# Kernel optimization log

Measured on AMD Instinct MI355X. Metric: run time of the kernel, lower is better.

The kernel has to match this reference:

```python
import jax, jax.numpy as jnp
import numpy as np

WD, WH, WW = 2, 7, 7          # window size (D, H, W)
SD, SH, SW = 1, 3, 3          # shift size
DIM, NH = 128, 4              # channels, heads
B, D, H, W = 8, 8, 56, 56     # input dims
N = WD * WH * WW              # tokens per window = 98
HIDDEN = int(DIM * 4.0)


def _rel_index_np():
    coords = np.stack(np.meshgrid(np.arange(WD), np.arange(WH), np.arange(WW), indexing='ij'))
    coords = coords.reshape(3, -1)                      # [3, N]
    rel = (coords[:, :, None] - coords[:, None, :]).transpose(1, 2, 0)  # [N, N, 3]
    rel[:, :, 0] += WD - 1
    rel[:, :, 1] += WH - 1
    rel[:, :, 2] += WW - 1
    rel[:, :, 0] *= (2 * WH - 1) * (2 * WW - 1)
    rel[:, :, 1] *= (2 * WW - 1)
    return rel.sum(-1).astype(np.int32)                 # [N, N]


def _window_partition_np(x):
    b, d, h, w, c = x.shape
    x = x.reshape(b, d // WD, WD, h // WH, WH, w // WW, WW, c)
    return x.transpose(0, 1, 3, 5, 2, 4, 6, 7).reshape(-1, N, c)


def _attn_mask_np():
    img = np.zeros((1, D, H, W, 1), np.float32)
    cnt = 0
    for ds in (slice(0, -WD), slice(-WD, -SD), slice(-SD, None)):
        for hs in (slice(0, -WH), slice(-WH, -SH), slice(-SH, None)):
            for ws in (slice(0, -WW), slice(-WW, -SW), slice(-SW, None)):
                img[:, ds, hs, ws, :] = cnt
                cnt += 1
    mw = _window_partition_np(img).reshape(-1, N)       # [nW, N]
    am = mw[:, None, :] - mw[:, :, None]
    return np.where(am != 0, -100.0, 0.0).astype(np.float32)  # [nW, N, N]


def setup_inputs() -> dict:
    key = jax.random.key(0)
    ks = jax.random.split(key, 8)
    s = 0.02
    return {
        'x': jax.random.normal(ks[0], (B, D, H, W, DIM), jnp.float32),
        'mask_matrix': jnp.asarray(_attn_mask_np()),
        'rel_index': jnp.asarray(_rel_index_np()),
        'norm1_g': jnp.ones((DIM,), jnp.float32),
        'norm1_b': jnp.zeros((DIM,), jnp.float32),
        'qkv_w': s * jax.random.normal(ks[1], (DIM, 3 * DIM), jnp.float32),
        'qkv_b': jnp.zeros((3 * DIM,), jnp.float32),
        'rpb': s * jax.random.normal(ks[2], ((2 * WD - 1) * (2 * WH - 1) * (2 * WW - 1), NH), jnp.float32),
        'proj_w': s * jax.random.normal(ks[3], (DIM, DIM), jnp.float32),
        'proj_b': jnp.zeros((DIM,), jnp.float32),
        'norm2_g': jnp.ones((DIM,), jnp.float32),
        'norm2_b': jnp.zeros((DIM,), jnp.float32),
        'fc1_w': s * jax.random.normal(ks[4], (DIM, HIDDEN), jnp.float32),
        'fc1_b': jnp.zeros((HIDDEN,), jnp.float32),
        'fc2_w': s * jax.random.normal(ks[5], (HIDDEN, DIM), jnp.float32),
        'fc2_b': jnp.zeros((DIM,), jnp.float32),
    }


def _ln(x, g, b):
    mu = jnp.mean(x, -1, keepdims=True)
    v = jnp.mean((x - mu) ** 2, -1, keepdims=True)
    return (x - mu) * jax.lax.rsqrt(v + 1e-5) * g + b


def _partition(x):
    b, d, h, w, c = x.shape
    x = x.reshape(b, d // WD, WD, h // WH, WH, w // WW, WW, c)
    return x.transpose(0, 1, 3, 5, 2, 4, 6, 7).reshape(-1, N, c)


def _reverse(win, b, d, h, w):
    c = win.shape[-1]
    x = win.reshape(b, d // WD, h // WH, w // WW, WD, WH, WW, c)
    return x.transpose(0, 1, 4, 2, 5, 3, 6, 7).reshape(b, d, h, w, c)


def _forward(x, mask_matrix, rel_index, norm1_g, norm1_b, qkv_w, qkv_b, rpb,
             proj_w, proj_b, norm2_g, norm2_b, fc1_w, fc1_b, fc2_w, fc2_b):
    b, d, h, w, c = x.shape
    shortcut = x
    y = _ln(x, norm1_g, norm1_b)
    # pad to multiples of window size (static; 0 for chosen dims)
    pd, ph, pw = (-d) % WD, (-h) % WH, (-w) % WW
    y = jnp.pad(y, ((0, 0), (0, pd), (0, ph), (0, pw), (0, 0)))
    dp, hp, wp = d + pd, h + ph, w + pw
    # cyclic shift
    y = jnp.roll(y, (-SD, -SH, -SW), axis=(1, 2, 3))
    win = _partition(y)                                   # [Bw, N, C]
    bw = win.shape[0]
    hd = c // NH
    qkv = (win @ qkv_w + qkv_b).reshape(bw, N, 3, NH, hd).transpose(2, 0, 3, 1, 4)
    q, k, v = qkv[0] * (hd ** -0.5), qkv[1], qkv[2]       # [Bw, NH, N, hd]
    attn = jnp.einsum('bhnd,bhmd->bhnm', q, k)            # [Bw, NH, N, N]
    bias = rpb[rel_index].transpose(2, 0, 1)              # [NH, N, N]
    attn = attn + bias[None]
    nw = mask_matrix.shape[0]
    attn = attn.reshape(bw // nw, nw, NH, N, N) + mask_matrix[None, :, None]
    attn = jax.nn.softmax(attn.reshape(bw, NH, N, N), axis=-1)
    o = jnp.einsum('bhnm,bhmd->bhnd', attn, v).transpose(0, 2, 1, 3).reshape(bw, N, c)
    o = o @ proj_w + proj_b
    y = _reverse(o, b, dp, hp, wp)
    y = jnp.roll(y, (SD, SH, SW), axis=(1, 2, 3))[:, :d, :h, :w, :]
    x1 = shortcut + y                                     # first residual
    z = _ln(x1, norm2_g, norm2_b)
    z = jax.nn.gelu(z @ fc1_w + fc1_b, approximate=False)
    # NOTE: source code's call() returns drop_path(mlp(norm2(x))) WITHOUT the
    # second residual add; we replicate exactly (drop_path is Identity at rate 0).
    return z @ fc2_w + fc2_b


def reference(x, mask_matrix, rel_index, norm1_g, norm1_b, qkv_w, qkv_b, rpb,
              proj_w, proj_b, norm2_g, norm2_b, fc1_w, fc1_b, fc2_w, fc2_b):
    return _forward(x, mask_matrix, rel_index, norm1_g, norm1_b, qkv_w, qkv_b,
                    rpb, proj_w, proj_b, norm2_g, norm2_b, fc1_w, fc1_b, fc2_w, fc2_b)


if __name__ == '__main__':
    out = reference(**setup_inputs())
    print(out.shape)
```

## Files before the change

### kernel.cpp

```cpp
#include <hip/hip_runtime.h>
#include <hip/hip_bf16.h>

typedef __attribute__((ext_vector_type(8))) short bf16x8;
typedef __attribute__((ext_vector_type(4))) float f32x4;

#define MFMA(a,b,c) __builtin_amdgcn_mfma_f32_16x16x32_bf16((a),(b),(c),0,0,0)
#define WAVE_LDS_FENCE() do { asm volatile("s_waitcnt lgkmcnt(0)" ::: "memory"); \
                              __builtin_amdgcn_sched_barrier(0); } while (0)

static constexpr int NTOK = 8 * 8 * 56 * 56;
static constexpr int NT   = 98;
static constexpr int NWIN = 2048;
static constexpr int NN   = NT * NT;

__device__ __forceinline__ unsigned short f2bf(float f) {
  unsigned r;
  asm("v_cvt_pk_bf16_f32 %0, %1, %1" : "=v"(r) : "v"(f));
  return (unsigned short)r;
}
__device__ __forceinline__ unsigned f2bf2(float lo, float hi) {
  unsigned r;
  asm("v_cvt_pk_bf16_f32 %0, %1, %2" : "=v"(r) : "v"(lo), "v"(hi));
  return r;
}
__device__ __forceinline__ float bf2f(unsigned short s) {
  union { unsigned u; float f; } v; v.u = ((unsigned)s) << 16; return v.f;
}
union U8 { unsigned u[4]; bf16x8 v; };

__device__ __forceinline__ size_t srow_of(int t) {
  int widx = t / NT, n = t - widx * NT;
  int bb = widx >> 8, wb = widx & 255;
  int dW = wb >> 6, hW = (wb >> 3) & 7, wW = wb & 7;
  int dr = n / 49, rem = n - dr * 49, hr = rem / 7, wr = rem - hr * 7;
  int dsh = (dW * 2 + dr + 1) & 7;
  int hs = hW * 7 + hr + 3; if (hs >= 56) hs -= 56;
  int wsv = wW * 7 + wr + 3; if (wsv >= 56) wsv -= 56;
  return ((size_t)(bb * 8 + dsh) * 56 + hs) * 56 + wsv;
}

__global__ __launch_bounds__(256) void k0_prep(
    const float* __restrict__ qkv_w, const float* __restrict__ proj_w,
    const float* __restrict__ fc1_w, const float* __restrict__ fc2_w,
    const float* __restrict__ n1g, const float* __restrict__ n1b,
    const float* __restrict__ qkv_b,
    unsigned short* __restrict__ qkvT, unsigned short* __restrict__ projT,
    unsigned short* __restrict__ fc1T, unsigned short* __restrict__ fc2T,
    float* __restrict__ qbb) {
  int idx = blockIdx.x * 256 + threadIdx.x;
  if (idx < 384 * 128) { int n = idx >> 7, k = idx & 127; qkvT[idx] = f2bf(qkv_w[k * 384 + n] * n1g[k]); }
  if (idx < 128 * 128) { int n = idx >> 7, k = idx & 127; projT[idx] = f2bf(proj_w[k * 128 + n]); }
  if (idx < 512 * 128) { int n = idx >> 7, k = idx & 127; fc1T[idx] = f2bf(fc1_w[k * 512 + n]); }
  if (idx < 128 * 512) { int n = idx >> 9, k = idx & 511; fc2T[idx] = f2bf(fc2_w[k * 128 + n]); }
  if (idx < 384) {
    float acc = qkv_b[idx];
    for (int k = 0; k < 128; ++k) acc += n1b[k] * qkv_w[k * 384 + idx];
    qbb[idx] = acc;
  }
}

__global__ __launch_bounds__(256) void k0b_cmb(
    const int* __restrict__ rel, const float* __restrict__ rpb,
    const float* __restrict__ mask, unsigned short* __restrict__ cmb) {
  int idx = blockIdx.x * 256 + threadIdx.x;
  if (idx >= 4 * 8 * NN) return;
  int h = idx / (8 * NN);
  int rem = idx - h * 8 * NN;
  int cls = rem / NN, r = rem - cls * NN;
  int wb_rep = ((cls >> 2) & 1 ? 192 : 0) + ((cls >> 1) & 1 ? 56 : 0) + ((cls & 1) ? 7 : 0);
  cmb[idx] = f2bf(rpb[rel[r] * 4 + h] + mask[(size_t)wb_rep * NN + r]);
}

__global__ __launch_bounds__(256, 2) void k2_qkv(
    const float* __restrict__ x, const unsigned short* __restrict__ qkvT,
    const float* __restrict__ qbb,
    unsigned short* __restrict__ q, unsigned short* __restrict__ k,
    unsigned short* __restrict__ v) {
  __shared__ __align__(16) unsigned short wsW[64 * 136];
  int tid = threadIdx.x, wv = tid >> 6, lane = tid & 63;
  int l15 = lane & 15, lhi = lane >> 4;
  int mbase = blockIdx.x * 128 + wv * 32;

  bf16x8 afr[2][4];
#pragma unroll
  for (int mt = 0; mt < 2; ++mt) {
    int row = mbase + mt * 16 + l15;
    size_t srow = srow_of(row);
    const float* xr = x + srow * 128 + lhi * 8;
    float xv[4][8];
    float s = 0.f, ss = 0.f;
#pragma unroll
    for (int ks = 0; ks < 4; ++ks) {
      float4 lo = *(const float4*)(xr + ks * 32);
      float4 hi = *(const float4*)(xr + ks * 32 + 4);
      xv[ks][0] = lo.x; xv[ks][1] = lo.y; xv[ks][2] = lo.z; xv[ks][3] = lo.w;
      xv[ks][4] = hi.x; xv[ks][5] = hi.y; xv[ks][6] = hi.z; xv[ks][7] = hi.w;
#pragma unroll
      for (int e = 0; e < 8; ++e) { s += xv[ks][e]; ss += xv[ks][e] * xv[ks][e]; }
    }
    s += __shfl_xor(s, 16);  ss += __shfl_xor(ss, 16);
    s += __shfl_xor(s, 32);  ss += __shfl_xor(ss, 32);
    float mu = s * (1.f / 128.f);
    float var = ss * (1.f / 128.f) - mu * mu;
    float inv = __builtin_amdgcn_rsqf(var + 1e-5f);
#pragma unroll
    for (int ks = 0; ks < 4; ++ks) {
      U8 t;
#pragma unroll
      for (int p = 0; p < 4; ++p)
        t.u[p] = f2bf2((xv[ks][2 * p] - mu) * inv, (xv[ks][2 * p + 1] - mu) * inv);
      afr[mt][ks] = t.v;
    }
  }

  int rbase[2][4];
#pragma unroll
  for (int mt = 0; mt < 2; ++mt)
#pragma unroll
    for (int j = 0; j < 4; ++j) {
      int r = mbase + mt * 16 + lhi * 4 + j;
      int widx = r / NT, n = r - widx * NT;
      rbase[mt][j] = widx * 392 + n;
    }

  bf16x8 pf[4];
#pragma unroll
  for (int u = 0; u < 4; ++u) pf[u] = *(const bf16x8*)(qkvT + u * 2048 + tid * 8);

  for (int ch = 0; ch < 6; ++ch) {
#pragma unroll
    for (int u = 0; u < 4; ++u) {
      int flat = u * 2048 + tid * 8;
      *(bf16x8*)(&wsW[(flat >> 7) * 136 + (flat & 127)]) = pf[u];
    }
    __syncthreads();
    if (ch < 5) {
#pragma unroll
      for (int u = 0; u < 4; ++u)
        pf[u] = *(const bf16x8*)(qkvT + (ch + 1) * 8192 + u * 2048 + tid * 8);
    }
    f32x4 acc[2][4] = {};
#pragma unroll
    for (int ks = 0; ks < 4; ++ks)
#pragma unroll
      for (int nt = 0; nt < 4; ++nt) {
        bf16x8 bfr = *(const bf16x8*)(&wsW[(nt * 16 + l15) * 136 + ks * 32 + lhi * 8]);
#pragma unroll
        for (int mt = 0; mt < 2; ++mt)
          acc[mt][nt] = MFMA(afr[mt][ks], bfr, acc[mt][nt]);
      }
#pragma unroll
    for (int nt = 0; nt < 4; ++nt) {
      int col = ch * 64 + nt * 16 + l15;
      int which = col >> 7, head = (col >> 5) & 3, hd = col & 31;
      unsigned short* outb = which == 0 ? q : (which == 1 ? k : v);
      float scale = which == 0 ? 0.17677669529663687f : 1.0f;
      float bias = qbb[col];
#pragma unroll
      for (int mt = 0; mt < 2; ++mt)
#pragma unroll
        for (int j = 0; j < 4; ++j) {
          float val = (acc[mt][nt][j] + bias) * scale;
          outb[(size_t)(rbase[mt][j] + head * 98) * 32 + hd] = f2bf(val);
        }
    }
    __syncthreads();
  }
}

__global__ __launch_bounds__(512) void k3_attn(
    const unsigned short* __restrict__ q, const unsigned short* __restrict__ kk,
    const unsigned short* __restrict__ vv, const unsigned short* __restrict__ cmb,
    unsigned short* __restrict__ out) {
  __shared__ __align__(16) unsigned short Vt[32 * 140];
  __shared__ __align__(16) unsigned short Pw[7][16 * 140];
  int bid = blockIdx.x;
  int widx = bid >> 2, head = bid & 3;
  int wb = widx & 255;
  size_t base = (size_t)(widx * 4 + head) * NT * 32;
  int tid = threadIdx.x, wv = tid >> 6, lane = tid & 63;
  int l15 = lane & 15, lhi = lane >> 4;

  for (int idx = tid; idx < NT * 32; idx += 512) {
    int j = idx >> 5, d = idx & 31;
    Vt[d * 140 + j] = vv[base + idx];
  }
  for (int idx = tid; idx < 32 * 30; idx += 512) {
    int d = idx / 30, j = 98 + idx % 30;
    Vt[d * 140 + j] = 0;
  }
  __syncthreads();
  if (wv >= 7) return;

  int cls = (((wb >> 6) == 3) << 2) | ((((wb >> 3) & 7) == 7) << 1) | ((int)((wb & 7) == 7));
  const unsigned short* cw = cmb + ((size_t)(head * 8 + cls)) * NN;
  unsigned short* P = Pw[wv];
  int mb = wv * 16;

  bf16x8 afr = *(const bf16x8*)(q + base + (size_t)(mb + l15) * 32 + lhi * 8);
  f32x4 sfr[7];
#pragma unroll
  for (int nt = 0; nt < 7; ++nt) {
    bf16x8 bfr = *(const bf16x8*)(kk + base + (size_t)(nt * 16 + l15) * 32 + lhi * 8);
    f32x4 zz = {};
    sfr[nt] = MFMA(afr, bfr, zz);
  }
#pragma unroll
  for (int j = 0; j < 4; ++j) {
    int i = mb + lhi * 4 + j;
    int ic = i < 97 ? i : 97;
    float sv[7];
#pragma unroll
    for (int nt = 0; nt < 7; ++nt) {
      int colc = nt * 16 + l15;
      int jc = colc < 97 ? colc : 97;
      float s = fminf(fmaxf(sfr[nt][j], -1e4f), 1e4f);
      float bm = bf2f(cw[ic * NT + jc]);
      sv[nt] = (i < NT && colc < NT) ? (s + bm) : -1e30f;
    }
    float mx = sv[0];
#pragma unroll
    for (int nt = 1; nt < 7; ++nt) mx = fmaxf(mx, sv[nt]);
#pragma unroll
    for (int m2 = 1; m2 < 16; m2 <<= 1) mx = fmaxf(mx, __shfl_xor(mx, m2));
    float sum = 0.f, p[7];
#pragma unroll
    for (int nt = 0; nt < 7; ++nt) { p[nt] = __expf(sv[nt] - mx); sum += p[nt]; }
#pragma unroll
    for (int m2 = 1; m2 < 16; m2 <<= 1) sum += __shfl_xor(sum, m2);
    float inv = __builtin_amdgcn_rcpf(sum);
    int iloc = lhi * 4 + j;
#pragma unroll
    for (int nt = 0; nt < 7; ++nt)
      P[iloc * 140 + nt * 16 + l15] = f2bf(p[nt] * inv);
    P[iloc * 140 + 112 + l15] = 0;
  }
  WAVE_LDS_FENCE();

  f32x4 ofr[2] = {};
#pragma unroll
  for (int ks = 0; ks < 4; ++ks) {
    bf16x8 pafr = *(const bf16x8*)(P + l15 * 140 + ks * 32 + lhi * 8);
#pragma unroll
    for (int nt = 0; nt < 2; ++nt) {
      bf16x8 bfr = *(const bf16x8*)(Vt + (nt * 16 + l15) * 140 + ks * 32 + lhi * 8);
      ofr[nt] = MFMA(pafr, bfr, ofr[nt]);
    }
  }
#pragma unroll
  for (int nt = 0; nt < 2; ++nt)
#pragma unroll
    for (int j = 0; j < 4; ++j) {
      int n = mb + lhi * 4 + j;
      if (n < NT) {
        int d = nt * 16 + l15;
        out[(size_t)(widx * NT + n) * 128 + head * 32 + d] = f2bf(ofr[nt][j]);
      }
    }
}

__global__ __launch_bounds__(256, 3) void k4_proj_ln(
    const unsigned short* __restrict__ ao, const unsigned short* __restrict__ projT,
    const float* __restrict__ proj_b, const float* __restrict__ x,
    const float* __restrict__ g2, const float* __restrict__ b2,
    unsigned short* __restrict__ z) {
  __shared__ __align__(16) unsigned short wsW[128 * 136];
  int tid = threadIdx.x, wv = tid >> 6, lane = tid & 63;
  int l15 = lane & 15, lhi = lane >> 4;
  int mbase = blockIdx.x * 128 + wv * 32;

#pragma unroll
  for (int u = 0; u < 8; ++u) {
    int flat = u * 2048 + tid * 8;
    *(bf16x8*)(&wsW[(flat >> 7) * 136 + (flat & 127)]) = *(const bf16x8*)(projT + flat);
  }
  bf16x8 afr[2][4];
#pragma unroll
  for (int mt = 0; mt < 2; ++mt)
#pragma unroll
    for (int ks = 0; ks < 4; ++ks)
      afr[mt][ks] = *(const bf16x8*)(ao + (size_t)(mbase + mt * 16 + l15) * 128 + ks * 32 + lhi * 8);
  __syncthreads();

  f32x4 acc[2][8] = {};
#pragma unroll
  for (int ks = 0; ks < 4; ++ks)
#pragma unroll
    for (int nt = 0; nt < 8; ++nt) {
      bf16x8 bfr = *(const bf16x8*)(&wsW[(nt * 16 + l15) * 136 + ks * 32 + lhi * 8]);
#pragma unroll
      for (int mt = 0; mt < 2; ++mt)
        acc[mt][nt] = MFMA(afr[mt][ks], bfr, acc[mt][nt]);
    }
  __syncthreads();

  float* bounce = (float*)wsW + wv * (16 * 132);
  float pb[8];
#pragma unroll
  for (int nt = 0; nt < 8; ++nt) pb[nt] = proj_b[nt * 16 + l15];

  int rl = lane >> 2, c0 = (lane & 3) * 32;
#pragma unroll
  for (int mt = 0; mt < 2; ++mt) {
#pragma unroll
    for (int nt = 0; nt < 8; ++nt)
#pragma unroll
      for (int j = 0; j < 4; ++j)
        bounce[(lhi * 4 + j) * 132 + nt * 16 + l15] = acc[mt][nt][j] + pb[nt];
    WAVE_LDS_FENCE();

    int t = mbase + mt * 16 + rl;
    size_t srow = srow_of(t);
    const float* xr = x + srow * 128 + c0;
    float vals[32];
    float s = 0.f, ss = 0.f;
#pragma unroll
    for (int i = 0; i < 8; ++i) {
      float4 pv = *(const float4*)(bounce + rl * 132 + c0 + 4 * i);
      float4 xv = *(const float4*)(xr + 4 * i);
      float a0 = pv.x + xv.x, a1 = pv.y + xv.y, a2 = pv.z + xv.z, a3 = pv.w + xv.w;
      vals[4 * i] = a0; vals[4 * i + 1] = a1; vals[4 * i + 2] = a2; vals[4 * i + 3] = a3;
      s += a0 + a1 + a2 + a3;
      ss += a0 * a0 + a1 * a1 + a2 * a2 + a3 * a3;
    }
    s += __shfl_xor(s, 1);  ss += __shfl_xor(ss, 1);
    s += __shfl_xor(s, 2);  ss += __shfl_xor(ss, 2);
    float mu = s * (1.f / 128.f);
    float var = ss * (1.f / 128.f) - mu * mu;
    float inv = __builtin_amdgcn_rsqf(var + 1e-5f);
    unsigned pk[16];
#pragma unroll
    for (int i = 0; i < 8; ++i) {
      float4 g = *(const float4*)(g2 + c0 + 4 * i);
      float4 b = *(const float4*)(b2 + c0 + 4 * i);
      pk[2 * i]     = f2bf2((vals[4 * i]     - mu) * inv * g.x + b.x,
                            (vals[4 * i + 1] - mu) * inv * g.y + b.y);
      pk[2 * i + 1] = f2bf2((vals[4 * i + 2] - mu) * inv * g.z + b.z,
                            (vals[4 * i + 3] - mu) * inv * g.w + b.w);
    }
    unsigned* zp = (unsigned*)(z + srow * 128 + c0);
#pragma unroll
    for (int i = 0; i < 4; ++i)
      *(uint4*)(zp + 4 * i) = make_uint4(pk[4 * i], pk[4 * i + 1], pk[4 * i + 2], pk[4 * i + 3]);
    WAVE_LDS_FENCE();
  }
}

__global__ __launch_bounds__(256, 2) void k5_mlp(
    const unsigned short* __restrict__ z, const unsigned short* __restrict__ fc1T,
    const float* __restrict__ fc1_b, const unsigned short* __restrict__ fc2T,
    const float* __restrict__ fc2_b, float* __restrict__ out) {
  __shared__ __align__(16) unsigned short wsA[64 * 132];
  __shared__ __align__(16) unsigned short wsB[128 * 68];
  __shared__ __align__(16) unsigned short hl[4][32 * 70];
  int tid = threadIdx.x, wv = tid >> 6, lane = tid & 63;
  int l15 = lane & 15, lhi = lane >> 4;
  int mbase = blockIdx.x * 128 + wv * 32;
  unsigned short* hw = hl[wv];

  bf16x8 afr[2][4];
#pragma unroll
  for (int mt = 0; mt < 2; ++mt)
#pragma unroll
    for (int ks = 0; ks < 4; ++ks)
      afr[mt][ks] = *(const bf16x8*)(z + (size_t)(mbase + mt * 16 + l15) * 128 + ks * 32 + lhi * 8);

  bf16x8 pfA[4], pfB[4];
#pragma unroll
  for (int u = 0; u < 4; ++u) pfA[u] = *(const bf16x8*)(fc1T + u * 2048 + tid * 8);
#pragma unroll
  for (int u = 0; u < 4; ++u) {
    int flat = u * 2048 + tid * 8;
    pfB[u] = *(const bf16x8*)(fc2T + (size_t)(flat >> 6) * 512 + (flat & 63));
  }

  f32x4 oacc[2][8] = {};
  for (int ch = 0; ch < 8; ++ch) {
#pragma unroll
    for (int u = 0; u < 4; ++u) {
      int flat = u * 2048 + tid * 8;
      *(bf16x8*)(&wsA[(flat >> 7) * 132 + (flat & 127)]) = pfA[u];
      *(bf16x8*)(&wsB[(flat >> 6) * 68 + (flat & 63)]) = pfB[u];
    }
    __syncthreads();
    if (ch < 7) {
#pragma unroll
      for (int u = 0; u < 4; ++u)
        pfA[u] = *(const bf16x8*)(fc1T + (ch + 1) * 8192 + u * 2048 + tid * 8);
#pragma unroll
      for (int u = 0; u < 4; ++u) {
        int flat = u * 2048 + tid * 8;
        pfB[u] = *(const bf16x8*)(fc2T + (size_t)(flat >> 6) * 512 + (ch + 1) * 64 + (flat & 63));
      }
    }
    f32x4 hacc[2][4] = {};
#pragma unroll
    for (int ks = 0; ks < 4; ++ks)
#pragma unroll
      for (int nt = 0; nt < 4; ++nt) {
        bf16x8 bfr = *(const bf16x8*)(&wsA[(nt * 16 + l15) * 132 + ks * 32 + lhi * 8]);
#pragma unroll
        for (int mt = 0; mt < 2; ++mt)
          hacc[mt][nt] = MFMA(afr[mt][ks], bfr, hacc[mt][nt]);
      }
#pragma unroll
    for (int mt = 0; mt < 2; ++mt)
#pragma unroll
      for (int nt = 0; nt < 4; ++nt)
#pragma unroll
        for (int j = 0; j < 4; ++j) {
          int r = mt * 16 + lhi * 4 + j;
          int hcol = ch * 64 + nt * 16 + l15;
          float hv = hacc[mt][nt][j] + fc1_b[hcol];
          float targ = hv * (1.5957691216f + 0.0713548162f * hv * hv);
          float gv = hv * __builtin_amdgcn_rcpf(1.0f + __expf(-targ));
          hw[r * 70 + nt * 16 + l15] = f2bf(gv);
        }
    WAVE_LDS_FENCE();
#pragma unroll
    for (int ks = 0; ks < 2; ++ks) {
      bf16x8 a2[2];
#pragma unroll
      for (int mt = 0; mt < 2; ++mt)
        a2[mt] = *(const bf16x8*)(&hw[(mt * 16 + l15) * 70 + ks * 32 + lhi * 8]);
#pragma unroll
      for (int nt = 0; nt < 8; ++nt) {
        bf16x8 bfr = *(const bf16x8*)(&wsB[(nt * 16 + l15) * 68 + ks * 32 + lhi * 8]);
#pragma unroll
        for (int mt = 0; mt < 2; ++mt)
          oacc[mt][nt] = MFMA(a2[mt], bfr, oacc[mt][nt]);
      }
    }
    WAVE_LDS_FENCE();
    __syncthreads();
  }
#pragma unroll
  for (int mt = 0; mt < 2; ++mt)
#pragma unroll
    for (int nt = 0; nt < 8; ++nt)
#pragma unroll
      for (int j = 0; j < 4; ++j) {
        int r = mbase + mt * 16 + lhi * 4 + j;
        out[(size_t)r * 128 + nt * 16 + l15] = oacc[mt][nt][j] + fc2_b[nt * 16 + l15];
      }
}

extern "C" void kernel_launch(void* const* d_in, const int* in_sizes, int n_in,
                              void* d_out, int out_size, void* d_ws, size_t ws_size,
                              hipStream_t stream) {
  const float* x      = (const float*)d_in[0];
  const float* mask   = (const float*)d_in[1];
  const int*   rel    = (const int*)d_in[2];
  const float* n1g    = (const float*)d_in[3];
  const float* n1b    = (const float*)d_in[4];
  const float* qkv_w  = (const float*)d_in[5];
  const float* qkv_b  = (const float*)d_in[6];
  const float* rpb    = (const float*)d_in[7];
  const float* proj_w = (const float*)d_in[8];
  const float* proj_b = (const float*)d_in[9];
  const float* n2g    = (const float*)d_in[10];
  const float* n2b    = (const float*)d_in[11];
  const float* fc1_w  = (const float*)d_in[12];
  const float* fc1_b  = (const float*)d_in[13];
  const float* fc2_w  = (const float*)d_in[14];
  const float* fc2_b  = (const float*)d_in[15];
  float* out = (float*)d_out;

  char* ws = (char*)d_ws;
  const size_t SZ = (size_t)NTOK * 128 * 2;
  unsigned short* win   = (unsigned short*)(ws);
  unsigned short* qb    = (unsigned short*)(ws + SZ);
  unsigned short* kb    = (unsigned short*)(ws + 2 * SZ);
  unsigned short* vb    = (unsigned short*)(ws + 3 * SZ);
  unsigned short* qkvT  = (unsigned short*)(ws + 4 * SZ);
  unsigned short* projT = qkvT + 384 * 128;
  unsigned short* fc1T  = projT + 128 * 128;
  unsigned short* fc2T  = fc1T + 512 * 128;
  unsigned short* cmb   = fc2T + 128 * 512;
  float* qbb            = (float*)(cmb + (size_t)4 * 8 * NN);
  unsigned short* ao = win;
  unsigned short* zb = qb;

  k0_prep<<<256, 256, 0, stream>>>(qkv_w, proj_w, fc1_w, fc2_w, n1g, n1b, qkv_b,
                                   qkvT, projT, fc1T, fc2T, qbb);
  k0b_cmb<<<(4 * 8 * NN + 255) / 256, 256, 0, stream>>>(rel, rpb, mask, cmb);
  k2_qkv<<<NTOK / 128, 256, 0, stream>>>(x, qkvT, qbb, qb, kb, vb);
  k3_attn<<<NWIN * 4, 512, 0, stream>>>(qb, kb, vb, cmb, ao);
  k4_proj_ln<<<NTOK / 128, 256, 0, stream>>>(ao, projT, proj_b, x, n2g, n2b, zb);
  k5_mlp<<<NTOK / 128, 256, 0, stream>>>(zb, fc1T, fc1_b, fc2T, fc2_b, out);
}
```

Measured before the change: 355.5 us.

## Fuse projection+LayerNorm kernel with MLP kernel, keeping LN output in LDS

Merges the attention projection/residual/LayerNorm kernel with the MLP kernel so the normalized activations are passed through LDS into MFMA fragments instead of being written to and reread from a global bf16 buffer. The final output is staged through LDS and written in the original token order. It also folds the query scale into the qkv weights and bias during prep, and splits the GELU/fc2 step into halves. This saves a global round trip and a kernel launch, but the fused kernel uses more LDS and registers, and occupancy bounds drop from 3 to 2 blocks.

New measurement: 478.9 us. 34.7% more time.

```diff
diff --git a/kernel.cpp b/kernel.cpp
--- a/kernel.cpp
+++ b/kernel.cpp
@@ -48,14 +48,18 @@
     unsigned short* __restrict__ fc1T, unsigned short* __restrict__ fc2T,
     float* __restrict__ qbb) {
   int idx = blockIdx.x * 256 + threadIdx.x;
-  if (idx < 384 * 128) { int n = idx >> 7, k = idx & 127; qkvT[idx] = f2bf(qkv_w[k * 384 + n] * n1g[k]); }
+  if (idx < 384 * 128) {
+    int n = idx >> 7, k = idx & 127;
+    float sc = n < 128 ? 0.17677669529663687f : 1.0f;
+    qkvT[idx] = f2bf(qkv_w[k * 384 + n] * n1g[k] * sc);
+  }
   if (idx < 128 * 128) { int n = idx >> 7, k = idx & 127; projT[idx] = f2bf(proj_w[k * 128 + n]); }
   if (idx < 512 * 128) { int n = idx >> 7, k = idx & 127; fc1T[idx] = f2bf(fc1_w[k * 512 + n]); }
   if (idx < 128 * 512) { int n = idx >> 9, k = idx & 511; fc2T[idx] = f2bf(fc2_w[k * 128 + n]); }
   if (idx < 384) {
     float acc = qkv_b[idx];
     for (int k = 0; k < 128; ++k) acc += n1b[k] * qkv_w[k * 384 + idx];
-    qbb[idx] = acc;
+    qbb[idx] = acc * (idx < 128 ? 0.17677669529663687f : 1.0f);
   }
 }
 
@@ -154,13 +158,12 @@
       int col = ch * 64 + nt * 16 + l15;
       int which = col >> 7, head = (col >> 5) & 3, hd = col & 31;
       unsigned short* outb = which == 0 ? q : (which == 1 ? k : v);
-      float scale = which == 0 ? 0.17677669529663687f : 1.0f;
       float bias = qbb[col];
 #pragma unroll
       for (int mt = 0; mt < 2; ++mt)
 #pragma unroll
         for (int j = 0; j < 4; ++j) {
-          float val = (acc[mt][nt][j] + bias) * scale;
+          float val = acc[mt][nt][j] + bias;
           outb[(size_t)(rbase[mt][j] + head * 98) * 32 + hd] = f2bf(val);
         }
     }
@@ -259,27 +262,31 @@
     }
 }
 
-__global__ __launch_bounds__(256, 3) void k4_proj_ln(
+__global__ __launch_bounds__(256, 2) void k45_proj_mlp(
     const unsigned short* __restrict__ ao, const unsigned short* __restrict__ projT,
     const float* __restrict__ proj_b, const float* __restrict__ x,
     const float* __restrict__ g2, const float* __restrict__ b2,
-    unsigned short* __restrict__ z) {
-  __shared__ __align__(16) unsigned short wsW[128 * 136];
+    const unsigned short* __restrict__ fc1T, const float* __restrict__ fc1_b,
+    const unsigned short* __restrict__ fc2T, const float* __restrict__ fc2_b,
+    float* __restrict__ out) {
+  __shared__ __align__(16) char smem[52224];
   int tid = threadIdx.x, wv = tid >> 6, lane = tid & 63;
   int l15 = lane & 15, lhi = lane >> 4;
   int mbase = blockIdx.x * 128 + wv * 32;
-
+  int rl = lane >> 2, c0 = (lane & 3) * 32;
+
+  unsigned short* wsW = (unsigned short*)smem;
 #pragma unroll
   for (int u = 0; u < 8; ++u) {
     int flat = u * 2048 + tid * 8;
     *(bf16x8*)(&wsW[(flat >> 7) * 136 + (flat & 127)]) = *(const bf16x8*)(projT + flat);
   }
-  bf16x8 afr[2][4];
+  bf16x8 aofr[2][4];
 #pragma unroll
   for (int mt = 0; mt < 2; ++mt)
 #pragma unroll
     for (int ks = 0; ks < 4; ++ks)
-      afr[mt][ks] = *(const bf16x8*)(ao + (size_t)(mbase + mt * 16 + l15) * 128 + ks * 32 + lhi * 8);
+      aofr[mt][ks] = *(const bf16x8*)(ao + (size_t)(mbase + mt * 16 + l15) * 128 + ks * 32 + lhi * 8);
   __syncthreads();
 
   f32x4 acc[2][8] = {};
@@ -290,33 +297,36 @@
       bf16x8 bfr = *(const bf16x8*)(&wsW[(nt * 16 + l15) * 136 + ks * 32 + lhi * 8]);
 #pragma unroll
       for (int mt = 0; mt < 2; ++mt)
-        acc[mt][nt] = MFMA(afr[mt][ks], bfr, acc[mt][nt]);
+        acc[mt][nt] = MFMA(aofr[mt][ks], bfr, acc[mt][nt]);
     }
   __syncthreads();
 
-  float* bounce = (float*)wsW + wv * (16 * 132);
+  float* bounce = (float*)(smem + wv * 8704);
+  unsigned short* zt = (unsigned short*)(smem + wv * 8704);
   float pb[8];
 #pragma unroll
   for (int nt = 0; nt < 8; ++nt) pb[nt] = proj_b[nt * 16 + l15];
 
-  int rl = lane >> 2, c0 = (lane & 3) * 32;
+  bf16x8 afr[2][4];
+  size_t srows[2];
 #pragma unroll
   for (int mt = 0; mt < 2; ++mt) {
 #pragma unroll
     for (int nt = 0; nt < 8; ++nt)
 #pragma unroll
       for (int j = 0; j < 4; ++j)
-        bounce[(lhi * 4 + j) * 132 + nt * 16 + l15] = acc[mt][nt][j] + pb[nt];
+        bounce[(lhi * 4 + j) * 136 + nt * 16 + l15] = acc[mt][nt][j] + pb[nt];
     WAVE_LDS_FENCE();
 
     int t = mbase + mt * 16 + rl;
     size_t srow = srow_of(t);
+    srows[mt] = srow;
     const float* xr = x + srow * 128 + c0;
     float vals[32];
     float s = 0.f, ss = 0.f;
 #pragma unroll
     for (int i = 0; i < 8; ++i) {
-      float4 pv = *(const float4*)(bounce + rl * 132 + c0 + 4 * i);
+      float4 pv = *(const float4*)(bounce + rl * 136 + c0 + 4 * i);
       float4 xv = *(const float4*)(xr + 4 * i);
       float a0 = pv.x + xv.x, a1 = pv.y + xv.y, a2 = pv.z + xv.z, a3 = pv.w + xv.w;
       vals[4 * i] = a0; vals[4 * i + 1] = a1; vals[4 * i + 2] = a2; vals[4 * i + 3] = a3;
@@ -338,32 +348,16 @@
       pk[2 * i + 1] = f2bf2((vals[4 * i + 2] - mu) * inv * g.z + b.z,
                             (vals[4 * i + 3] - mu) * inv * g.w + b.w);
     }
-    unsigned* zp = (unsigned*)(z + srow * 128 + c0);
-#pragma unroll
-    for (int i = 0; i < 4; ++i)
-      *(uint4*)(zp + 4 * i) = make_uint4(pk[4 * i], pk[4 * i + 1], pk[4 * i + 2], pk[4 * i + 3]);
-    WAVE_LDS_FENCE();
-  }
-}
-
-__global__ __launch_bounds__(256, 2) void k5_mlp(
-    const unsigned short* __restrict__ z, const unsigned short* __restrict__ fc1T,
-    const float* __restrict__ fc1_b, const unsigned short* __restrict__ fc2T,
-    const float* __restrict__ fc2_b, float* __restrict__ out) {
-  __shared__ __align__(16) unsigned short wsA[64 * 132];
-  __shared__ __align__(16) unsigned short wsB[128 * 68];
-  __shared__ __align__(16) unsigned short hl[4][32 * 70];
-  int tid = threadIdx.x, wv = tid >> 6, lane = tid & 63;
-  int l15 = lane & 15, lhi = lane >> 4;
-  int mbase = blockIdx.x * 128 + wv * 32;
-  unsigned short* hw = hl[wv];
-
-  bf16x8 afr[2][4];
-#pragma unroll
-  for (int mt = 0; mt < 2; ++mt)
+    WAVE_LDS_FENCE();
+#pragma unroll
+    for (int i = 0; i < 16; ++i)
+      *(unsigned*)(zt + rl * 136 + c0 + 2 * i) = pk[i];
+    WAVE_LDS_FENCE();
 #pragma unroll
     for (int ks = 0; ks < 4; ++ks)
-      afr[mt][ks] = *(const bf16x8*)(z + (size_t)(mbase + mt * 16 + l15) * 128 + ks * 32 + lhi * 8);
+      afr[mt][ks] = *(const bf16x8*)(zt + l15 * 136 + ks * 32 + lhi * 8);
+    WAVE_LDS_FENCE();
+  }
 
   bf16x8 pfA[4], pfB[4];
 #pragma unroll
@@ -373,6 +367,11 @@
     int flat = u * 2048 + tid * 8;
     pfB[u] = *(const bf16x8*)(fc2T + (size_t)(flat >> 6) * 512 + (flat & 63));
   }
+  __syncthreads();
+
+  unsigned short* wsA = (unsigned short*)smem;
+  unsigned short* wsB = wsA + 64 * 132;
+  unsigned short* hw  = wsB + 128 * 68 + wv * (32 * 70);
 
   f32x4 oacc[2][8] = {};
   for (int ch = 0; ch < 8; ++ch) {
@@ -404,45 +403,55 @@
           hacc[mt][nt] = MFMA(afr[mt][ks], bfr, hacc[mt][nt]);
       }
 #pragma unroll
-    for (int mt = 0; mt < 2; ++mt)
-#pragma unroll
-      for (int nt = 0; nt < 4; ++nt)
-#pragma unroll
-        for (int j = 0; j < 4; ++j) {
-          int r = mt * 16 + lhi * 4 + j;
-          int hcol = ch * 64 + nt * 16 + l15;
-          float hv = hacc[mt][nt][j] + fc1_b[hcol];
-          float targ = hv * (1.5957691216f + 0.0713548162f * hv * hv);
-          float gv = hv * __builtin_amdgcn_rcpf(1.0f + __expf(-targ));
-          hw[r * 70 + nt * 16 + l15] = f2bf(gv);
+    for (int half = 0; half < 2; ++half) {
+#pragma unroll
+      for (int mt = 0; mt < 2; ++mt)
+#pragma unroll
+        for (int nt2 = 0; nt2 < 2; ++nt2) {
+          int nt = half * 2 + nt2;
+#pragma unroll
+          for (int j = 0; j < 4; ++j) {
+            int r = mt * 16 + lhi * 4 + j;
+            int hcol = ch * 64 + nt * 16 + l15;
+            float hv = hacc[mt][nt][j] + fc1_b[hcol];
+            float targ = hv * (1.5957691216f + 0.0713548162f * hv * hv);
+            float gv = hv * __builtin_amdgcn_rcpf(1.0f + __expf(-targ));
+            hw[r * 70 + nt * 16 + l15] = f2bf(gv);
+          }
         }
-    WAVE_LDS_FENCE();
-#pragma unroll
-    for (int ks = 0; ks < 2; ++ks) {
       bf16x8 a2[2];
 #pragma unroll
       for (int mt = 0; mt < 2; ++mt)
-        a2[mt] = *(const bf16x8*)(&hw[(mt * 16 + l15) * 70 + ks * 32 + lhi * 8]);
+        a2[mt] = *(const bf16x8*)(&hw[(mt * 16 + l15) * 70 + half * 32 + lhi * 8]);
 #pragma unroll
       for (int nt = 0; nt < 8; ++nt) {
-        bf16x8 bfr = *(const bf16x8*)(&wsB[(nt * 16 + l15) * 68 + ks * 32 + lhi * 8]);
+        bf16x8 bfr = *(const bf16x8*)(&wsB[(nt * 16 + l15) * 68 + half * 32 + lhi * 8]);
 #pragma unroll
         for (int mt = 0; mt < 2; ++mt)
           oacc[mt][nt] = MFMA(a2[mt], bfr, oacc[mt][nt]);
       }
     }
-    WAVE_LDS_FENCE();
     __syncthreads();
   }
-#pragma unroll
-  for (int mt = 0; mt < 2; ++mt)
+
+  float* ob = (float*)(smem + wv * 8704);
+  float fb[8];
+#pragma unroll
+  for (int nt = 0; nt < 8; ++nt) fb[nt] = fc2_b[nt * 16 + l15];
+#pragma unroll
+  for (int mt = 0; mt < 2; ++mt) {
 #pragma unroll
     for (int nt = 0; nt < 8; ++nt)
 #pragma unroll
-      for (int j = 0; j < 4; ++j) {
-        int r = mbase + mt * 16 + lhi * 4 + j;
-        out[(size_t)r * 128 + nt * 16 + l15] = oacc[mt][nt][j] + fc2_b[nt * 16 + l15];
-      }
+      for (int j = 0; j < 4; ++j)
+        ob[(lhi * 4 + j) * 136 + nt * 16 + l15] = oacc[mt][nt][j] + fb[nt];
+    WAVE_LDS_FENCE();
+    float* orow = out + srows[mt] * 128 + c0;
+#pragma unroll
+    for (int i = 0; i < 8; ++i)
+      *(float4*)(orow + 4 * i) = *(const float4*)(ob + rl * 136 + c0 + 4 * i);
+    WAVE_LDS_FENCE();
+  }
 }
 
 extern "C" void kernel_launch(void* const* d_in, const int* in_sizes, int n_in,
@@ -479,13 +488,12 @@
   unsigned short* cmb   = fc2T + 128 * 512;
   float* qbb            = (float*)(cmb + (size_t)4 * 8 * NN);
   unsigned short* ao = win;
-  unsigned short* zb = qb;
 
   k0_prep<<<256, 256, 0, stream>>>(qkv_w, proj_w, fc1_w, fc2_w, n1g, n1b, qkv_b,
                                    qkvT, projT, fc1T, fc2T, qbb);
   k0b_cmb<<<(4 * 8 * NN + 255) / 256, 256, 0, stream>>>(rel, rpb, mask, cmb);
   k2_qkv<<<NTOK / 128, 256, 0, stream>>>(x, qkvT, qbb, qb, kb, vb);
   k3_attn<<<NWIN * 4, 512, 0, stream>>>(qb, kb, vb, cmb, ao);
-  k4_proj_ln<<<NTOK / 128, 256, 0, stream>>>(ao, projT, proj_b, x, n2g, n2b, zb);
-  k5_mlp<<<NTOK / 128, 256, 0, stream>>>(zb, fc1T, fc1_b, fc2T, fc2_b, out);
-}
+  k45_proj_mlp<<<NTOK / 128, 256, 0, stream>>>(ao, projT, proj_b, x, n2g, n2b,
+                                               fc1T, fc1_b, fc2T, fc2_b, out);
+}
```

## Pre-permute bias+mask table for vector loads, fold q scale into weights, prefetch residual

Applied to the files above, without the earlier changes.

The combined relative-position-bias and mask table is rebuilt in a lane-major padded layout (98x128 per head/class), so each lane in the attention kernel loads its seven bias values with one 16-byte vector load instead of seven scattered scalar loads. The attention query scale is folded into the prepared QKV weights and bias, which removes a multiply per output in the QKV kernel. The projection+LayerNorm kernel now issues the residual x loads early, before the GEMM, to hide their latency. The cost is slightly larger bias storage and more registers held live in k4.

Measured after the change: 352.8 us. No clear change (-0.7%).

```diff
diff --git a/kernel.cpp b/kernel.cpp
--- a/kernel.cpp
+++ b/kernel.cpp
@@ -48,14 +48,18 @@
     unsigned short* __restrict__ fc1T, unsigned short* __restrict__ fc2T,
     float* __restrict__ qbb) {
   int idx = blockIdx.x * 256 + threadIdx.x;
-  if (idx < 384 * 128) { int n = idx >> 7, k = idx & 127; qkvT[idx] = f2bf(qkv_w[k * 384 + n] * n1g[k]); }
+  if (idx < 384 * 128) {
+    int n = idx >> 7, k = idx & 127;
+    float sc = n < 128 ? 0.17677669529663687f : 1.0f;
+    qkvT[idx] = f2bf(qkv_w[k * 384 + n] * n1g[k] * sc);
+  }
   if (idx < 128 * 128) { int n = idx >> 7, k = idx & 127; projT[idx] = f2bf(proj_w[k * 128 + n]); }
   if (idx < 512 * 128) { int n = idx >> 7, k = idx & 127; fc1T[idx] = f2bf(fc1_w[k * 512 + n]); }
   if (idx < 128 * 512) { int n = idx >> 9, k = idx & 511; fc2T[idx] = f2bf(fc2_w[k * 128 + n]); }
   if (idx < 384) {
     float acc = qkv_b[idx];
     for (int k = 0; k < 128; ++k) acc += n1b[k] * qkv_w[k * 384 + idx];
-    qbb[idx] = acc;
+    qbb[idx] = acc * (idx < 128 ? 0.17677669529663687f : 1.0f);
   }
 }
 
@@ -63,12 +67,20 @@
     const int* __restrict__ rel, const float* __restrict__ rpb,
     const float* __restrict__ mask, unsigned short* __restrict__ cmb) {
   int idx = blockIdx.x * 256 + threadIdx.x;
-  if (idx >= 4 * 8 * NN) return;
-  int h = idx / (8 * NN);
-  int rem = idx - h * 8 * NN;
-  int cls = rem / NN, r = rem - cls * NN;
-  int wb_rep = ((cls >> 2) & 1 ? 192 : 0) + ((cls >> 1) & 1 ? 56 : 0) + ((cls & 1) ? 7 : 0);
-  cmb[idx] = f2bf(rpb[rel[r] * 4 + h] + mask[(size_t)wb_rep * NN + r]);
+  if (idx >= 4 * 8 * 98 * 128) return;
+  int nt = idx & 7;
+  int l15 = (idx >> 3) & 15;
+  int rest = idx >> 7;
+  int i = rest % 98;
+  int hc = rest / 98;
+  int h = hc >> 3, cls = hc & 7;
+  int col = nt * 16 + l15;
+  float val = 0.f;
+  if (nt < 7 && col < 98) {
+    int wb_rep = ((cls >> 2) & 1 ? 192 : 0) + ((cls >> 1) & 1 ? 56 : 0) + ((cls & 1) ? 7 : 0);
+    val = rpb[rel[i * NT + col] * 4 + h] + mask[(size_t)wb_rep * NN + i * NT + col];
+  }
+  cmb[idx] = f2bf(val);
 }
 
 __global__ __launch_bounds__(256, 2) void k2_qkv(
@@ -154,13 +166,12 @@
       int col = ch * 64 + nt * 16 + l15;
       int which = col >> 7, head = (col >> 5) & 3, hd = col & 31;
       unsigned short* outb = which == 0 ? q : (which == 1 ? k : v);
-      float scale = which == 0 ? 0.17677669529663687f : 1.0f;
       float bias = qbb[col];
 #pragma unroll
       for (int mt = 0; mt < 2; ++mt)
 #pragma unroll
         for (int j = 0; j < 4; ++j) {
-          float val = (acc[mt][nt][j] + bias) * scale;
+          float val = acc[mt][nt][j] + bias;
           outb[(size_t)(rbase[mt][j] + head * 98) * 32 + hd] = f2bf(val);
         }
     }
@@ -193,7 +204,7 @@
   if (wv >= 7) return;
 
   int cls = (((wb >> 6) == 3) << 2) | ((((wb >> 3) & 7) == 7) << 1) | ((int)((wb & 7) == 7));
-  const unsigned short* cw = cmb + ((size_t)(head * 8 + cls)) * NN;
+  const unsigned short* cw = cmb + (size_t)(head * 8 + cls) * 98 * 128;
   unsigned short* P = Pw[wv];
   int mb = wv * 16;
 
@@ -209,13 +220,13 @@
   for (int j = 0; j < 4; ++j) {
     int i = mb + lhi * 4 + j;
     int ic = i < 97 ? i : 97;
+    bf16x8 cv = *(const bf16x8*)(cw + ic * 128 + l15 * 8);
     float sv[7];
 #pragma unroll
     for (int nt = 0; nt < 7; ++nt) {
       int colc = nt * 16 + l15;
-      int jc = colc < 97 ? colc : 97;
       float s = fminf(fmaxf(sfr[nt][j], -1e4f), 1e4f);
-      float bm = bf2f(cw[ic * NT + jc]);
+      float bm = bf2f((unsigned short)cv[nt]);
       sv[nt] = (i < NT && colc < NT) ? (s + bm) : -1e30f;
     }
     float mx = sv[0];
@@ -268,6 +279,15 @@
   int tid = threadIdx.x, wv = tid >> 6, lane = tid & 63;
   int l15 = lane & 15, lhi = lane >> 4;
   int mbase = blockIdx.x * 128 + wv * 32;
+  int rl = lane >> 2, c0 = (lane & 3) * 32;
+
+  size_t srows[2];
+  srows[0] = srow_of(mbase + rl);
+  srows[1] = srow_of(mbase + 16 + rl);
+  float4 x0[8];
+#pragma unroll
+  for (int i = 0; i < 8; ++i)
+    x0[i] = *(const float4*)(x + srows[0] * 128 + c0 + 4 * i);
 
 #pragma unroll
   for (int u = 0; u < 8; ++u) {
@@ -294,12 +314,16 @@
     }
   __syncthreads();
 
+  float4 x1[8];
+#pragma unroll
+  for (int i = 0; i < 8; ++i)
+    x1[i] = *(const float4*)(x + srows[1] * 128 + c0 + 4 * i);
+
   float* bounce = (float*)wsW + wv * (16 * 132);
   float pb[8];
 #pragma unroll
   for (int nt = 0; nt < 8; ++nt) pb[nt] = proj_b[nt * 16 + l15];
 
-  int rl = lane >> 2, c0 = (lane & 3) * 32;
 #pragma unroll
   for (int mt = 0; mt < 2; ++mt) {
 #pragma unroll
@@ -309,15 +333,13 @@
         bounce[(lhi * 4 + j) * 132 + nt * 16 + l15] = acc[mt][nt][j] + pb[nt];
     WAVE_LDS_FENCE();
 
-    int t = mbase + mt * 16 + rl;
-    size_t srow = srow_of(t);
-    const float* xr = x + srow * 128 + c0;
+    size_t srow = srows[mt];
     float vals[32];
     float s = 0.f, ss = 0.f;
 #pragma unroll
     for (int i = 0; i < 8; ++i) {
       float4 pv = *(const float4*)(bounce + rl * 132 + c0 + 4 * i);
-      float4 xv = *(const float4*)(xr + 4 * i);
+      float4 xv = mt == 0 ? x0[i] : x1[i];
       float a0 = pv.x + xv.x, a1 = pv.y + xv.y, a2 = pv.z + xv.z, a3 = pv.w + xv.w;
       vals[4 * i] = a0; vals[4 * i + 1] = a1; vals[4 * i + 2] = a2; vals[4 * i + 3] = a3;
       s += a0 + a1 + a2 + a3;
@@ -477,13 +499,13 @@
   unsigned short* fc1T  = projT + 128 * 128;
   unsigned short* fc2T  = fc1T + 512 * 128;
   unsigned short* cmb   = fc2T + 128 * 512;
-  float* qbb            = (float*)(cmb + (size_t)4 * 8 * NN);
+  float* qbb            = (float*)(cmb + (size_t)4 * 8 * 98 * 128);
   unsigned short* ao = win;
   unsigned short* zb = qb;
 
   k0_prep<<<256, 256, 0, stream>>>(qkv_w, proj_w, fc1_w, fc2_w, n1g, n1b, qkv_b,
                                    qkvT, projT, fc1T, fc2T, qbb);
-  k0b_cmb<<<(4 * 8 * NN + 255) / 256, 256, 0, stream>>>(rel, rpb, mask, cmb);
+  k0b_cmb<<<(4 * 8 * 98 * 128 + 255) / 256, 256, 0, stream>>>(rel, rpb, mask, cmb);
   k2_qkv<<<NTOK / 128, 256, 0, stream>>>(x, qkvT, qbb, qb, kb, vb);
   k3_attn<<<NWIN * 4, 512, 0, stream>>>(qb, kb, vb, cmb, ao);
   k4_proj_ln<<<NTOK / 128, 256, 0, stream>>>(ao, projT, proj_b, x, n2g, n2b, zb);
```
